# Performance work log

Measured on AMD Instinct MI355X. Metric: run time of the kernel, lower is better.

The kernel has to match this reference:

```python
import jax, jax.numpy as jnp
import numpy as np

NEG_INF = -1e9
LRELU_SLOPE = 0.2  # torch GAT default leaky_relu negative slope


def setup_inputs() -> dict:
    key = jax.random.key(0)
    k1, k2, k3, k4, k5 = jax.random.split(key, 5)
    N, F_IN, H, DH = 4096, 1433, 8, 8  # n_nodes, in_features, n_heads, per-head dim (n_hidden=64)
    vert = jax.random.normal(k1, (N, F_IN), dtype=jnp.float32)
    edge = jax.random.randint(k2, (N, N), 0, 2, dtype=jnp.int32)  # dense adjacency mask
    W = jax.random.normal(k3, (F_IN, H * DH), dtype=jnp.float32) * 0.05
    a_l = jax.random.normal(k4, (H, DH), dtype=jnp.float32) * 0.05
    a_r = jax.random.normal(k5, (H, DH), dtype=jnp.float32) * 0.05
    return {"vert": vert, "edge": edge, "W": W, "a_l": a_l, "a_r": a_r}


def reference(vert, edge, W, a_l, a_r):
    # GAT-style edge-affinity layer (is_concat=True) + ELU; dropout is identity (eval mode).
    N = vert.shape[0]
    H, DH = a_l.shape
    g = (vert @ W).reshape(N, H, DH)                      # [N,H,Dh] projected node features
    sl = jnp.einsum('nhd,hd->nh', g, a_l)                 # source-node attention term
    sr = jnp.einsum('nhd,hd->nh', g, a_r)                 # target-node attention term
    e = sl[:, None, :] + sr[None, :, :]                   # [N,N,H]: attn([g_i || g_j])
    e = jnp.where(e >= 0, e, LRELU_SLOPE * e)             # leaky_relu
    mask = (edge != 0)[:, :, None]                        # [N,N,1]
    e = jnp.where(mask, e, NEG_INF)                       # mask non-edges
    a = jax.nn.softmax(e, axis=1)                         # normalize over neighbors j
    out = jnp.einsum('ijh,jhd->ihd', a, g).reshape(N, H * DH)  # aggregate + concat heads
    return jax.nn.elu(out)
```

## Files before the change

### kernel.cpp

```cpp
#include <hip/hip_runtime.h>
#include <hip/hip_bf16.h>

#define NN 4096
#define FIN 1433
#define NH 8
#define DH 8
#define HD 64
#define KP 1472
#define LOG2E 1.44269504f
#define NJS 8
#define NCHK ((NN / NJS) / 128)

typedef unsigned int u32;
typedef unsigned long long u64;
typedef float v4f __attribute__((ext_vector_type(4)));
typedef _Float16 f16;
typedef _Float16 h2 __attribute__((ext_vector_type(2)));
typedef _Float16 f16x8 __attribute__((ext_vector_type(8)));

static __device__ __forceinline__ short f2h16(float f) {
    union { f16 h; short s; } u; u.h = (f16)f; return u.s;
}
static __device__ __forceinline__ h2 u2h2(u32 x) {
    union { u32 u; h2 h; } v; v.u = x; return v.h;
}
static __device__ __forceinline__ u32 h22u(h2 x) {
    union { h2 h; u32 u; } v; v.h = x; return v.u;
}

#if __has_builtin(__builtin_amdgcn_sbfe)
#define SBFE1(x, k) __builtin_amdgcn_sbfe((int)(x), (k), 1)
#else
#define SBFE1(x, k) (((int)((x) << (31 - (k)))) >> 31)
#endif

__global__ __launch_bounds__(256) void k_wprep(const float* __restrict__ W,
                                               short* __restrict__ Wt) {
    __shared__ float Ts[64][65];
    const int c = blockIdx.x;
    const int u = threadIdx.x;
    const int n4 = (u & 15) * 4;
    const int kr = u >> 4;
#pragma unroll
    for (int q = 0; q < 4; ++q) {
        const int kl = kr + q * 16;
        const int kg = c * 64 + kl;
        v4f v = {0.f, 0.f, 0.f, 0.f};
        if (kg < FIN) v = *(const v4f*)&W[(size_t)kg * HD + n4];
        *(v4f*)&Ts[kl][n4] = v;
    }
    __syncthreads();
    const int n = u >> 2;
    const int koff = (u & 3) * 16;
    __align__(16) short tmp[16];
#pragma unroll
    for (int r = 0; r < 16; ++r) tmp[r] = f2h16(Ts[koff + r][n]);
    *(uint4*)&Wt[(size_t)n * KP + c * 64 + koff]     = *(uint4*)&tmp[0];
    *(uint4*)&Wt[(size_t)n * KP + c * 64 + koff + 8] = *(uint4*)&tmp[8];
}

__global__ __launch_bounds__(256, 4) void k_gemm(
    const float* __restrict__ vert, const short* __restrict__ Wt,
    const float* __restrict__ al, const float* __restrict__ ar,
    short* __restrict__ gT, short* __restrict__ eB, short* __restrict__ eD,
    float* __restrict__ Rw)
{
    __shared__ float cacc[4][16][64];

    const int t = threadIdx.x, lane = t & 63, w = t >> 6;
    const int ml = lane & 15, q = lane >> 4;
    const int i0 = blockIdx.x * 16;
    const float* vrow = vert + (size_t)(i0 + ml) * FIN;

    v4f acc[4];
#pragma unroll
    for (int g = 0; g < 4; ++g) acc[g] = (v4f){0.f, 0.f, 0.f, 0.f};

    for (int c = w; c < 45; c += 4) {
        const int k0 = c * 32 + q * 8;
        v4f a0, a1;
        if (k0 + 7 < FIN) {
            a0 = *(const v4f*)&vrow[k0];
            a1 = *(const v4f*)&vrow[k0 + 4];
        } else {
            float tmp[8];
#pragma unroll
            for (int e = 0; e < 8; ++e)
                tmp[e] = (k0 + e < FIN) ? vrow[k0 + e] : 0.f;
            a0 = (v4f){tmp[0], tmp[1], tmp[2], tmp[3]};
            a1 = (v4f){tmp[4], tmp[5], tmp[6], tmp[7]};
        }
        const f16x8 af = {(f16)a0.x, (f16)a0.y, (f16)a0.z, (f16)a0.w,
                          (f16)a1.x, (f16)a1.y, (f16)a1.z, (f16)a1.w};
#pragma unroll
        for (int g = 0; g < 4; ++g) {
            const f16x8 bf = *(const f16x8*)&Wt[(size_t)(g * 16 + ml) * KP + k0];
            acc[g] = __builtin_amdgcn_mfma_f32_16x16x32_f16(af, bf, acc[g], 0, 0, 0);
        }
    }

#pragma unroll
    for (int g = 0; g < 4; ++g)
#pragma unroll
        for (int r = 0; r < 4; ++r)
            cacc[w][q * 4 + r][g * 16 + ml] = acc[g][r];
    __syncthreads();

    const int m = t >> 4, n4 = (t & 15) * 4;
    v4f s = (v4f){0.f, 0.f, 0.f, 0.f};
#pragma unroll
    for (int ww = 0; ww < 4; ++ww) s += *(const v4f*)&cacc[ww][m][n4];

#pragma unroll
    for (int e = 0; e < 4; ++e)
        gT[(size_t)(n4 + e) * NN + i0 + m] = f2h16(s[e]);

    float pl = s.x * al[n4] + s.y * al[n4 + 1] + s.z * al[n4 + 2] + s.w * al[n4 + 3];
    float pr = s.x * ar[n4] + s.y * ar[n4 + 1] + s.z * ar[n4 + 2] + s.w * ar[n4 + 3];
    pl += __shfl_xor(pl, 1, 64);
    pr += __shfl_xor(pr, 1, 64);
    if ((t & 1) == 0) {
        const int h = (t & 15) >> 1;
        const int node = i0 + m;
        eB[h * NN + node] = f2h16(exp2f(pr * LOG2E));
        eD[h * NN + node] = f2h16(exp2f(0.2f * pr * LOG2E));
        Rw[node * NH + h] = exp2f(-0.8f * pl * LOG2E);
    }
}

__global__ __launch_bounds__(256, 4) void k_attn(
    const int* __restrict__ edge, const short* __restrict__ gT,
    const short* __restrict__ eB, const short* __restrict__ eD,
    const float* __restrict__ Rw,
    float* __restrict__ num, float* __restrict__ den)
{
    __shared__ __align__(16) short Gt[2][33][136];
    __shared__ __align__(16) short sB[2][4][136];
    __shared__ __align__(16) short sD[2][4][136];
    __shared__ u32 mA[2][64][4];
    __shared__ u32 mB[2][64][4];

    const int t = threadIdx.x, lane = t & 63, w = t >> 6;
    const int ml = lane & 15, quad = lane >> 4;
    const int i0 = blockIdx.x * 64;
    const int hg = blockIdx.y, js = blockIdx.z;
    const int jbase = js * (NN / NJS);
    const int h = hg * 4 + w;

    h2 Ri[4];
#pragma unroll
    for (int it = 0; it < 4; ++it) {
        const f16 rh = (f16)Rw[(i0 + it * 16 + ml) * NH + h];
        Ri[it] = (h2){rh, rh};
    }

    if (t < 136) { Gt[0][32][t] = 0x3C00; Gt[1][32][t] = 0x3C00; }

    const short* gTh = gT + (hg * 32) * NN;
    const short* eBh = eB + (hg * 4) * NN;
    const short* eDh = eD + (hg * 4) * NN;

    const int grow = t >> 3, gseg = (t & 7) * 16;
    const int bh = (t >> 4) & 3, bseg = (t & 15) * 8;

    {
        const int j0 = jbase;
        const uint4 g0 = *(const uint4*)&gTh[grow * NN + j0 + gseg];
        const uint4 g1 = *(const uint4*)&gTh[grow * NN + j0 + gseg + 8];
        *(uint4*)&Gt[0][grow][gseg]     = g0;
        *(uint4*)&Gt[0][grow][gseg + 8] = g1;
        if (t < 64)       *(uint4*)&sB[0][bh][bseg] = *(const uint4*)&eBh[bh * NN + j0 + bseg];
        else if (t < 128) *(uint4*)&sD[0][bh][bseg] = *(const uint4*)&eDh[bh * NN + j0 + bseg];
#pragma unroll
        for (int rr = 0; rr < 16; ++rr) {
            const int row = w * 16 + rr;
            const int2 e2 = *(const int2*)&edge[(i0 + row) * NN + j0 + 2 * lane];
            const u64 bA = __ballot(e2.x != 0);
            const u64 bB = __ballot(e2.y != 0);
            if (lane == 0)  { mA[0][row][0] = (u32)bA;         mB[0][row][0] = (u32)bB; }
            if (lane == 32) { mA[0][row][1] = (u32)(bA >> 32); mB[0][row][1] = (u32)(bB >> 32); }
        }
    }
    __syncthreads();

    v4f acc[4];
#pragma unroll
    for (int it = 0; it < 4; ++it) acc[it] = (v4f){0.f, 0.f, 0.f, 0.f};

    const int qb4 = quad * 4;
    const int browv = (ml < 8) ? (w * 8 + ml) : 32;

    for (int c = 0; c < NCHK; ++c) {
        const int cb = c & 1, nb = cb ^ 1;
        const bool pf = (c + 1) < NCHK;
        uint4 pg0, pg1, pb, pd; int2 pe[8];
        if (pf) {
            const int j0 = jbase + (c + 1) * 128;
            pg0 = *(const uint4*)&gTh[grow * NN + j0 + gseg];
            pg1 = *(const uint4*)&gTh[grow * NN + j0 + gseg + 8];
            if (t < 64)       pb = *(const uint4*)&eBh[bh * NN + j0 + bseg];
            else if (t < 128) pd = *(const uint4*)&eDh[bh * NN + j0 + bseg];
#pragma unroll
            for (int rr = 0; rr < 8; ++rr)
                pe[rr] = *(const int2*)&edge[(i0 + w * 16 + rr) * NN + j0 + 2 * lane];
        }
        uint2 wa[4], wb[4];
#pragma unroll
        for (int it = 0; it < 4; ++it) {
            wa[it] = *(const uint2*)&mA[cb][it * 16 + ml][0];
            wb[it] = *(const uint2*)&mB[cb][it * 16 + ml][0];
        }
#pragma unroll
        for (int s = 0; s < 4; ++s) {
            const uint4 bu = *(const uint4*)&sB[cb][w][s * 32 + quad * 8];
            const uint4 du = *(const uint4*)&sD[cb][w][s * 32 + quad * 8];
            const uint4 gu = *(const uint4*)&Gt[cb][browv][s * 32 + quad * 8];
            union { uint4 u; f16x8 h; } gub; gub.u = gu;
            const f16x8 bfrag = gub.h;
            const int base = ((s & 1) << 4) + qb4;
#pragma unroll
            for (int it = 0; it < 4; ++it) {
                const u32 WA = ((s >> 1) ? wa[it].y : wa[it].x) >> base;
                const u32 WB = ((s >> 1) ? wb[it].y : wb[it].x) >> base;
                u32 aw[4];
#pragma unroll
                for (int k = 0; k < 4; ++k) {
                    const int ea = SBFE1(WA, k);
                    const int eb = SBFE1(WB, k);
                    const u32 m = __builtin_amdgcn_perm((u32)eb, (u32)ea, 0x05040100u);
                    const u32 dk = (&du.x)[k];
                    const u32 bk = (&bu.x)[k];
                    const u32 rd = h22u(Ri[it] * u2h2(dk));
                    u32 pm;
                    asm("v_pk_max_f16 %0, %1, %2" : "=v"(pm) : "v"(rd), "v"(bk));
                    aw[k] = pm & m;
                }
                union { uint4 u; f16x8 h; } aub;
                aub.u = (uint4){aw[0], aw[1], aw[2], aw[3]};
                acc[it] = __builtin_amdgcn_mfma_f32_16x16x32_f16(aub.h, bfrag, acc[it], 0, 0, 0);
            }
        }
        if (pf) {
            const int j0 = jbase + (c + 1) * 128;
            *(uint4*)&Gt[nb][grow][gseg]     = pg0;
            *(uint4*)&Gt[nb][grow][gseg + 8] = pg1;
            if (t < 64)       *(uint4*)&sB[nb][bh][bseg] = pb;
            else if (t < 128) *(uint4*)&sD[nb][bh][bseg] = pd;
#pragma unroll
            for (int rr = 0; rr < 8; ++rr) {
                const int row = w * 16 + rr;
                const u64 bA = __ballot(pe[rr].x != 0);
                const u64 bB = __ballot(pe[rr].y != 0);
                if (lane == 0)  { mA[nb][row][0] = (u32)bA;         mB[nb][row][0] = (u32)bB; }
                if (lane == 32) { mA[nb][row][1] = (u32)(bA >> 32); mB[nb][row][1] = (u32)(bB >> 32); }
            }
#pragma unroll
            for (int rr = 8; rr < 16; ++rr) {
                const int row = w * 16 + rr;
                const int2 e2 = *(const int2*)&edge[(i0 + row) * NN + j0 + 2 * lane];
                const u64 bA = __ballot(e2.x != 0);
                const u64 bB = __ballot(e2.y != 0);
                if (lane == 0)  { mA[nb][row][0] = (u32)bA;         mB[nb][row][0] = (u32)bB; }
                if (lane == 32) { mA[nb][row][1] = (u32)(bA >> 32); mB[nb][row][1] = (u32)(bB >> 32); }
            }
        }
        __syncthreads();
    }

#pragma unroll
    for (int it = 0; it < 4; ++it) {
        const int ibase = i0 + it * 16 + quad * 4;
#pragma unroll
        for (int r = 0; r < 4; ++r) {
            if (ml < 8)       atomicAdd(&num[(ibase + r) * HD + h * 8 + ml], acc[it][r]);
            else if (ml == 8) atomicAdd(&den[(ibase + r) * NH + h], acc[it][r]);
        }
    }
}

__global__ __launch_bounds__(256) void k_comb(
    const float* __restrict__ num, const float* __restrict__ den,
    float* __restrict__ out)
{
    const int gid = blockIdx.x * 256 + threadIdx.x;
    const float x = num[gid] / den[(gid >> 6) * NH + ((gid >> 3) & 7)];
    out[gid] = (x > 0.f) ? x : (__expf(x) - 1.f);
}

extern "C" void kernel_launch(void* const* d_in, const int* in_sizes, int n_in,
                              void* d_out, int out_size, void* d_ws, size_t ws_size,
                              hipStream_t stream) {
    const float* vert = (const float*)d_in[0];
    const int*   edge = (const int*)d_in[1];
    const float* W    = (const float*)d_in[2];
    const float* al   = (const float*)d_in[3];
    const float* ar   = (const float*)d_in[4];
    float* out = (float*)d_out;

    char* ws = (char*)d_ws;
    short* gT  = (short*)ws;
    short* eB  = (short*)(ws + 512 * 1024);
    short* eD  = (short*)(ws + 576 * 1024);
    float* Rw  = (float*)(ws + 640 * 1024);
    short* Wt  = (short*)(ws + 768 * 1024);
    float* num = (float*)(ws + 1024 * 1024);
    float* den = (float*)(ws + 2048 * 1024);

    hipLaunchKernelGGL(k_wprep, dim3(23), dim3(256), 0, stream, W, Wt);
    hipLaunchKernelGGL(k_gemm, dim3(NN / 16), dim3(256), 0, stream,
                       vert, Wt, al, ar, gT, eB, eD, Rw);
    hipMemsetAsync(num, 0, (NN * HD + NN * NH) * sizeof(float), stream);
    hipLaunchKernelGGL(k_attn, dim3(NN / 64, 2, NJS), dim3(256), 0, stream,
                       edge, gT, eB, eD, Rw, num, den);
    hipLaunchKernelGGL(k_comb, dim3(NN * HD / 256), dim3(256), 0, stream,
                       num, den, out);
}
```

Before: 172.3 us.

## Shrink attention row tile, halve j-splits, replace atomics with per-split partials

The attention kernel now handles 32 query rows per block instead of 64 and splits the neighbor dimension into 4 slices instead of 8. Each slice writes its partial numerator and denominator to its own workspace region rather than using atomicAdd, and the combine kernel sums the slices. This removes the memset and the atomic contention. It also shortens the per-chunk edge-mask loading, since each warp now handles 8 rows. In exchange, each Gt/eB/eD tile is reused across fewer rows, so more redundant loads of the projected features are needed per edge, and each block runs longer, serial chunk loops.

```diff
diff --git a/kernel.cpp b/kernel.cpp
--- a/kernel.cpp
+++ b/kernel.cpp
@@ -8,7 +8,7 @@
 #define HD 64
 #define KP 1472
 #define LOG2E 1.44269504f
-#define NJS 8
+#define NJS 4
 #define NCHK ((NN / NJS) / 128)
 
 typedef unsigned int u32;
@@ -132,24 +132,24 @@
     const int* __restrict__ edge, const short* __restrict__ gT,
     const short* __restrict__ eB, const short* __restrict__ eD,
     const float* __restrict__ Rw,
-    float* __restrict__ num, float* __restrict__ den)
+    float* __restrict__ numw, float* __restrict__ denw)
 {
     __shared__ __align__(16) short Gt[2][33][136];
     __shared__ __align__(16) short sB[2][4][136];
     __shared__ __align__(16) short sD[2][4][136];
-    __shared__ u32 mA[2][64][4];
-    __shared__ u32 mB[2][64][4];
+    __shared__ u32 mA[2][32][4];
+    __shared__ u32 mB[2][32][4];
 
     const int t = threadIdx.x, lane = t & 63, w = t >> 6;
     const int ml = lane & 15, quad = lane >> 4;
-    const int i0 = blockIdx.x * 64;
+    const int i0 = blockIdx.x * 32;
     const int hg = blockIdx.y, js = blockIdx.z;
     const int jbase = js * (NN / NJS);
     const int h = hg * 4 + w;
 
-    h2 Ri[4];
-#pragma unroll
-    for (int it = 0; it < 4; ++it) {
+    h2 Ri[2];
+#pragma unroll
+    for (int it = 0; it < 2; ++it) {
         const f16 rh = (f16)Rw[(i0 + it * 16 + ml) * NH + h];
         Ri[it] = (h2){rh, rh};
     }
@@ -161,7 +161,7 @@
     const short* eDh = eD + (hg * 4) * NN;
 
     const int grow = t >> 3, gseg = (t & 7) * 16;
-    const int bh = (t >> 4) & 3, bseg = (t & 15) * 8;
+    const int bh = (t >> 3) & 3, bseg = (t & 7) * 16;
 
     {
         const int j0 = jbase;
@@ -169,11 +169,16 @@
         const uint4 g1 = *(const uint4*)&gTh[grow * NN + j0 + gseg + 8];
         *(uint4*)&Gt[0][grow][gseg]     = g0;
         *(uint4*)&Gt[0][grow][gseg + 8] = g1;
-        if (t < 64)       *(uint4*)&sB[0][bh][bseg] = *(const uint4*)&eBh[bh * NN + j0 + bseg];
-        else if (t < 128) *(uint4*)&sD[0][bh][bseg] = *(const uint4*)&eDh[bh * NN + j0 + bseg];
-#pragma unroll
-        for (int rr = 0; rr < 16; ++rr) {
-            const int row = w * 16 + rr;
+        if (t < 32) {
+            *(uint4*)&sB[0][bh][bseg]     = *(const uint4*)&eBh[bh * NN + j0 + bseg];
+            *(uint4*)&sB[0][bh][bseg + 8] = *(const uint4*)&eBh[bh * NN + j0 + bseg + 8];
+        } else if (t < 64) {
+            *(uint4*)&sD[0][bh][bseg]     = *(const uint4*)&eDh[bh * NN + j0 + bseg];
+            *(uint4*)&sD[0][bh][bseg + 8] = *(const uint4*)&eDh[bh * NN + j0 + bseg + 8];
+        }
+#pragma unroll
+        for (int rr = 0; rr < 8; ++rr) {
+            const int row = w * 8 + rr;
             const int2 e2 = *(const int2*)&edge[(i0 + row) * NN + j0 + 2 * lane];
             const u64 bA = __ballot(e2.x != 0);
             const u64 bB = __ballot(e2.y != 0);
@@ -183,9 +188,9 @@
     }
     __syncthreads();
 
-    v4f acc[4];
-#pragma unroll
-    for (int it = 0; it < 4; ++it) acc[it] = (v4f){0.f, 0.f, 0.f, 0.f};
+    v4f acc[2];
+    acc[0] = (v4f){0.f, 0.f, 0.f, 0.f};
+    acc[1] = (v4f){0.f, 0.f, 0.f, 0.f};
 
     const int qb4 = quad * 4;
     const int browv = (ml < 8) ? (w * 8 + ml) : 32;
@@ -193,20 +198,25 @@
     for (int c = 0; c < NCHK; ++c) {
         const int cb = c & 1, nb = cb ^ 1;
         const bool pf = (c + 1) < NCHK;
-        uint4 pg0, pg1, pb, pd; int2 pe[8];
+        uint4 pg0, pg1, pbd0, pbd1; int2 pe[8];
         if (pf) {
             const int j0 = jbase + (c + 1) * 128;
             pg0 = *(const uint4*)&gTh[grow * NN + j0 + gseg];
             pg1 = *(const uint4*)&gTh[grow * NN + j0 + gseg + 8];
-            if (t < 64)       pb = *(const uint4*)&eBh[bh * NN + j0 + bseg];
-            else if (t < 128) pd = *(const uint4*)&eDh[bh * NN + j0 + bseg];
+            if (t < 32) {
+                pbd0 = *(const uint4*)&eBh[bh * NN + j0 + bseg];
+                pbd1 = *(const uint4*)&eBh[bh * NN + j0 + bseg + 8];
+            } else if (t < 64) {
+                pbd0 = *(const uint4*)&eDh[bh * NN + j0 + bseg];
+                pbd1 = *(const uint4*)&eDh[bh * NN + j0 + bseg + 8];
+            }
 #pragma unroll
             for (int rr = 0; rr < 8; ++rr)
-                pe[rr] = *(const int2*)&edge[(i0 + w * 16 + rr) * NN + j0 + 2 * lane];
-        }
-        uint2 wa[4], wb[4];
-#pragma unroll
-        for (int it = 0; it < 4; ++it) {
+                pe[rr] = *(const int2*)&edge[(i0 + w * 8 + rr) * NN + j0 + 2 * lane];
+        }
+        uint2 wa[2], wb[2];
+#pragma unroll
+        for (int it = 0; it < 2; ++it) {
             wa[it] = *(const uint2*)&mA[cb][it * 16 + ml][0];
             wb[it] = *(const uint2*)&mB[cb][it * 16 + ml][0];
         }
@@ -219,7 +229,7 @@
             const f16x8 bfrag = gub.h;
             const int base = ((s & 1) << 4) + qb4;
 #pragma unroll
-            for (int it = 0; it < 4; ++it) {
+            for (int it = 0; it < 2; ++it) {
                 const u32 WA = ((s >> 1) ? wa[it].y : wa[it].x) >> base;
                 const u32 WB = ((s >> 1) ? wb[it].y : wb[it].x) >> base;
                 u32 aw[4];
@@ -228,11 +238,9 @@
                     const int ea = SBFE1(WA, k);
                     const int eb = SBFE1(WB, k);
                     const u32 m = __builtin_amdgcn_perm((u32)eb, (u32)ea, 0x05040100u);
-                    const u32 dk = (&du.x)[k];
-                    const u32 bk = (&bu.x)[k];
-                    const u32 rd = h22u(Ri[it] * u2h2(dk));
+                    const u32 rd = h22u(Ri[it] * u2h2((&du.x)[k]));
                     u32 pm;
-                    asm("v_pk_max_f16 %0, %1, %2" : "=v"(pm) : "v"(rd), "v"(bk));
+                    asm("v_pk_max_f16 %0, %1, %2" : "=v"(pm) : "v"(rd), "v"((&bu.x)[k]));
                     aw[k] = pm & m;
                 }
                 union { uint4 u; f16x8 h; } aub;
@@ -241,49 +249,53 @@
             }
         }
         if (pf) {
-            const int j0 = jbase + (c + 1) * 128;
             *(uint4*)&Gt[nb][grow][gseg]     = pg0;
             *(uint4*)&Gt[nb][grow][gseg + 8] = pg1;
-            if (t < 64)       *(uint4*)&sB[nb][bh][bseg] = pb;
-            else if (t < 128) *(uint4*)&sD[nb][bh][bseg] = pd;
+            if (t < 32) {
+                *(uint4*)&sB[nb][bh][bseg]     = pbd0;
+                *(uint4*)&sB[nb][bh][bseg + 8] = pbd1;
+            } else if (t < 64) {
+                *(uint4*)&sD[nb][bh][bseg]     = pbd0;
+                *(uint4*)&sD[nb][bh][bseg + 8] = pbd1;
+            }
 #pragma unroll
             for (int rr = 0; rr < 8; ++rr) {
-                const int row = w * 16 + rr;
+                const int row = w * 8 + rr;
                 const u64 bA = __ballot(pe[rr].x != 0);
                 const u64 bB = __ballot(pe[rr].y != 0);
                 if (lane == 0)  { mA[nb][row][0] = (u32)bA;         mB[nb][row][0] = (u32)bB; }
                 if (lane == 32) { mA[nb][row][1] = (u32)(bA >> 32); mB[nb][row][1] = (u32)(bB >> 32); }
             }
-#pragma unroll
-            for (int rr = 8; rr < 16; ++rr) {
-                const int row = w * 16 + rr;
-                const int2 e2 = *(const int2*)&edge[(i0 + row) * NN + j0 + 2 * lane];
-                const u64 bA = __ballot(e2.x != 0);
-                const u64 bB = __ballot(e2.y != 0);
-                if (lane == 0)  { mA[nb][row][0] = (u32)bA;         mB[nb][row][0] = (u32)bB; }
-                if (lane == 32) { mA[nb][row][1] = (u32)(bA >> 32); mB[nb][row][1] = (u32)(bB >> 32); }
-            }
         }
         __syncthreads();
     }
 
-#pragma unroll
-    for (int it = 0; it < 4; ++it) {
+    float* nw = numw + (size_t)js * NN * HD;
+    float* dw = denw + (size_t)js * NN * NH;
+#pragma unroll
+    for (int it = 0; it < 2; ++it) {
         const int ibase = i0 + it * 16 + quad * 4;
 #pragma unroll
         for (int r = 0; r < 4; ++r) {
-            if (ml < 8)       atomicAdd(&num[(ibase + r) * HD + h * 8 + ml], acc[it][r]);
-            else if (ml == 8) atomicAdd(&den[(ibase + r) * NH + h], acc[it][r]);
+            if (ml < 8)       nw[(ibase + r) * HD + h * 8 + ml] = acc[it][r];
+            else if (ml == 8) dw[(ibase + r) * NH + h]          = acc[it][r];
         }
     }
 }
 
 __global__ __launch_bounds__(256) void k_comb(
-    const float* __restrict__ num, const float* __restrict__ den,
+    const float* __restrict__ numw, const float* __restrict__ denw,
     float* __restrict__ out)
 {
     const int gid = blockIdx.x * 256 + threadIdx.x;
-    const float x = num[gid] / den[(gid >> 6) * NH + ((gid >> 3) & 7)];
+    const int i = gid >> 6, h = (gid & 63) >> 3;
+    float num = 0.f, den = 0.f;
+#pragma unroll
+    for (int s = 0; s < NJS; ++s) {
+        num += numw[s * NN * HD + gid];
+        den += denw[s * NN * NH + i * NH + h];
+    }
+    float x = num / den;
     out[gid] = (x > 0.f) ? x : (__expf(x) - 1.f);
 }
 
@@ -298,20 +310,19 @@
     float* out = (float*)d_out;
 
     char* ws = (char*)d_ws;
-    short* gT  = (short*)ws;
-    short* eB  = (short*)(ws + 512 * 1024);
-    short* eD  = (short*)(ws + 576 * 1024);
-    float* Rw  = (float*)(ws + 640 * 1024);
-    short* Wt  = (short*)(ws + 768 * 1024);
-    float* num = (float*)(ws + 1024 * 1024);
-    float* den = (float*)(ws + 2048 * 1024);
+    short* gT   = (short*)ws;
+    short* eB   = (short*)(ws + 512 * 1024);
+    short* eD   = (short*)(ws + 576 * 1024);
+    float* Rw   = (float*)(ws + 640 * 1024);
+    short* Wt   = (short*)(ws + 768 * 1024);
+    float* numw = (float*)(ws + 1024 * 1024);
+    float* denw = (float*)(ws + 5 * 1024 * 1024);
 
     hipLaunchKernelGGL(k_wprep, dim3(23), dim3(256), 0, stream, W, Wt);
     hipLaunchKernelGGL(k_gemm, dim3(NN / 16), dim3(256), 0, stream,
                        vert, Wt, al, ar, gT, eB, eD, Rw);
-    hipMemsetAsync(num, 0, (NN * HD + NN * NH) * sizeof(float), stream);
-    hipLaunchKernelGGL(k_attn, dim3(NN / 64, 2, NJS), dim3(256), 0, stream,
-                       edge, gT, eB, eD, Rw, num, den);
+    hipLaunchKernelGGL(k_attn, dim3(NN / 32, 2, NJS), dim3(256), 0, stream,
+                       edge, gT, eB, eD, Rw, numw, denw);
     hipLaunchKernelGGL(k_comb, dim3(NN * HD / 256), dim3(256), 0, stream,
-                       num, den, out);
-}
+                       numw, denw, out);
+}
```

After: 150.6 us. -12.6%, faster.
